# Performance work log

Hardware: AMD Instinct MI355X
Metric: run time of the kernel (lower is better)

Reference implementation:

```python
import jax, jax.numpy as jnp
import numpy as np
import math

B, CF, H, W = 2, 64, 256, 256
CH = 32          # 'channel' init arg
KS, DIL, PAD = 3, 2, 2
IMG_H, IMG_W = 512, 512


def _pos_encode(h, w, d_model):
    # Sinusoidal encoding along x and y, interleaved sin/cos -> [2*d_model, h, w]
    div = jnp.exp(jnp.arange(0, d_model, 2, dtype=jnp.float32) * (-math.log(10000.0) / d_model))  # [d/2]
    ax = jnp.arange(w, dtype=jnp.float32)[None, :] * div[:, None]   # [d/2, w]
    ay = jnp.arange(h, dtype=jnp.float32)[None, :] * div[:, None]   # [d/2, h]
    x = jnp.stack([jnp.sin(ax), jnp.cos(ax)], axis=1).reshape(d_model, w)  # even=sin, odd=cos
    y = jnp.stack([jnp.sin(ay), jnp.cos(ay)], axis=1).reshape(d_model, h)
    x = jnp.broadcast_to(x[:, None, :], (d_model, h, w))
    y = jnp.broadcast_to(y[:, :, None], (d_model, h, w))
    return jnp.concatenate([x, y], axis=0)  # [2*d_model, h, w]


def _unfold3x3(x):
    # F.unfold(kernel=3, dilation=2, padding=2, stride=1) -> [B, C, 9, H, W]
    b, c, h, w = x.shape
    xp = jnp.pad(x, ((0, 0), (0, 0), (PAD, PAD), (PAD, PAD)))
    offs = (0, DIL, 2 * DIL)
    patches = [xp[:, :, i:i + h, j:j + w] for i in offs for j in offs]  # row-major kernel order
    return jnp.stack(patches, axis=2)


def setup_inputs() -> dict:
    key = jax.random.key(0)
    k1, k2, k3, k4, k5 = jax.random.split(key, 5)
    return {
        "inp": jax.random.normal(k1, (B, CF, H, W), dtype=jnp.float32),
        "img": jax.random.uniform(k2, (B, 3, IMG_H, IMG_W), dtype=jnp.float32),
        "w_pos": jax.random.normal(k3, (CH, 2 * CH), dtype=jnp.float32) * 0.1,
        "w_img": jax.random.normal(k4, (CH, 3), dtype=jnp.float32) * 0.1,
        "w_comp": jax.random.normal(k5, (CF,), dtype=jnp.float32) * 0.1,
    }


def reference(inp, img, w_pos, w_img, w_comp):
    b, cf, h, w = inp.shape
    # positional embedding -> 1x1 conv (channel matmul)
    pos = _pos_encode(h, w, CH)                                   # [2*CH, H, W]
    pos_embd = jnp.einsum('oc,chw->ohw', w_pos, pos)              # [CH, H, W]
    pos_embd = jnp.broadcast_to(pos_embd[None], (b, CH, h, w))
    # bilinear resize of image to feature resolution, then 1x1 conv
    rimg = jax.image.resize(img, (b, 3, h, w), method='bilinear')
    rimg = jnp.einsum('oc,bchw->bohw', w_img, rimg)               # [B, CH, H, W]
    em = jnp.concatenate([rimg, pos_embd], axis=1)                # [B, 2*CH, H, W]
    # neighborhood similarity score
    un_em = _unfold3x3(em)                                        # [B, 2CH, 9, H, W]
    feature_score = jnp.einsum('bckhw,bchw->bkhw', un_em, em)     # [B, 9, H, W]
    # feature compatibility: 1x1 conv (dot with w_comp) per neighbor, sigmoid
    un_fea = _unfold3x3(inp)                                      # [B, CF, 9, H, W]
    comp_score = jax.nn.sigmoid(jnp.einsum('bckhw,c->bkhw', un_fea, w_comp))
    phi = comp_score * feature_score                              # [B, 9, H, W]
    weighted_fea = jnp.einsum('bckhw,bkhw->bchw', un_fea, phi)    # [B, CF, H, W]
    return weighted_fea
```

## Files before the change

### kernel.cpp

```cpp
#include <hip/hip_runtime.h>
#include <math.h>

namespace {
constexpr int Bn = 2, CF = 64;
constexpr int H = 256, W = 256, HW = H * W;
constexpr int IH = 512, IW = 512;

constexpr int OFF_MT   = 0;
constexpr int OFF_GXX  = OFF_MT + 256 * 256;
constexpr int OFF_GYY  = OFF_GXX + 3 * 256;
constexpr int OFF_G    = OFF_GYY + 3 * 256;
constexpr int OFF_RIMG = OFF_G + 16;
constexpr int OFF_S    = OFF_RIMG + Bn * 3 * HW;
constexpr int OFF_PX   = OFF_S + Bn * HW;
constexpr int OFF_PY   = OFF_PX + 32 * 256;

constexpr int GRAM_BLOCKS = 256;
constexpr int RIMG_BLOCKS = Bn * 3 * (HW / 256);
constexpr int SIGS_BLOCKS = Bn * (HW / 256);
constexpr int PREP_BLOCKS = GRAM_BLOCKS + RIMG_BLOCKS + SIGS_BLOCKS;
}

__global__ __launch_bounds__(256) void pxy_kernel(
    const float* __restrict__ w_pos,
    float* __restrict__ PX, float* __restrict__ PY)
{
  const int t = threadIdx.x;
  const int o = blockIdx.x;
  float s[16], c[16];
#pragma unroll
  for (int i = 0; i < 16; i++) {
    float d = expf((float)(2 * i) * (-0.2878231366242557f));
    float a = (float)t * d;
    s[i] = sinf(a);
    c[i] = cosf(a);
  }
  const float* wr = w_pos + o * 64;
  float ax = 0.f, ay = 0.f;
#pragma unroll
  for (int i = 0; i < 16; i++) {
    ax += wr[2 * i] * s[i] + wr[2 * i + 1] * c[i];
    ay += wr[32 + 2 * i] * s[i] + wr[33 + 2 * i] * c[i];
  }
  PX[o * 256 + t] = ax;
  PY[o * 256 + t] = ay;
}

__device__ __forceinline__ void resize_taps(int p, int n, float w[4], int idx[4])
{
#pragma unroll
  for (int r = 0; r < 4; r++) {
    int q = 2 * p - 1 + r;
    idx[r] = min(max(q, 0), 2 * n - 1);
  }
  if (p == 0)          { w[0] = 0.f;        w[1] = 3.f / 7.f; w[2] = 3.f / 7.f; w[3] = 1.f / 7.f; }
  else if (p == n - 1) { w[0] = 1.f / 7.f;  w[1] = 3.f / 7.f; w[2] = 3.f / 7.f; w[3] = 0.f; }
  else                 { w[0] = 0.125f;     w[1] = 0.375f;    w[2] = 0.375f;    w[3] = 0.125f; }
}

__global__ __launch_bounds__(256) void prep_kernel(
    const float* __restrict__ img, const float* __restrict__ inp,
    const float* __restrict__ w_comp, const float* __restrict__ w_img,
    const float* __restrict__ PX, const float* __restrict__ PY,
    float* __restrict__ rimg, float* __restrict__ sigs,
    float* __restrict__ Mt, float* __restrict__ GXX, float* __restrict__ GYY,
    float* __restrict__ G)
{
  __shared__ float4 red4[256];
  const int gid = blockIdx.x;

  if (gid < GRAM_BLOCKS) {
    const int a = threadIdx.x;
    const int t = gid;

    float m = 0.f;
#pragma unroll
    for (int o = 0; o < 32; o++) m += PX[o * 256 + a] * PY[o * 256 + t];
    Mt[t * 256 + a] = m;

    if (t == 0) {
#pragma unroll
      for (int j = 0; j < 3; j++) {
        const int nb = a + 2 * (j - 1);
        float gx = 0.f, gy = 0.f;
        if (nb >= 0 && nb < 256) {
#pragma unroll
          for (int o = 0; o < 32; o++) {
            gx += PX[o * 256 + a] * PX[o * 256 + nb];
            gy += PY[o * 256 + a] * PY[o * 256 + nb];
          }
        }
        GXX[j * 256 + a] = gx;
        GYY[j * 256 + a] = gy;
      }
      if (a < 9) {
        const int i = a / 3, j = a % 3;
        float g = 0.f;
#pragma unroll
        for (int o = 0; o < 32; o++) g += w_img[o * 3 + i] * w_img[o * 3 + j];
        G[a] = g;
      }
    }
  } else if (gid < GRAM_BLOCKS + RIMG_BLOCKS) {
    const int rid = gid - GRAM_BLOCKS;
    const int b = rid / 768;
    const int rem = rid % 768;
    const int c = rem / 256;
    const int p = (rem % 256) * 256 + threadIdx.x;
    const int x = p & (W - 1);
    const int y = p >> 8;

    float wy[4], wx[4];
    int ry[4], rx[4];
    resize_taps(y, H, wy, ry);
    resize_taps(x, W, wx, rx);

    const float* ip = img + ((size_t)(b * 3 + c) * IH) * IW;
    float acc = 0.f;
#pragma unroll
    for (int r = 0; r < 4; r++) {
      const float* rowp = ip + ry[r] * IW;
      float rs = wx[0] * rowp[rx[0]] + wx[1] * rowp[rx[1]] +
                 wx[2] * rowp[rx[2]] + wx[3] * rowp[rx[3]];
      acc += wy[r] * rs;
    }
    rimg[((size_t)(b * 3 + c)) * HW + p] = acc;
  } else {
    const int sid = gid - (GRAM_BLOCKS + RIMG_BLOCKS);
    const int b = sid / (HW / 256);
    const int pblk = sid % (HW / 256);
    const int lane = threadIdx.x & 63;
    const int cg = threadIdx.x >> 6;
    const int p0 = pblk * 256 + lane * 4;

    const float* ib = inp + (size_t)b * CF * HW + (size_t)cg * 16 * HW + p0;
    float4 acc = {0.f, 0.f, 0.f, 0.f};
#pragma unroll
    for (int c = 0; c < 16; c++) {
      const float4 v = *reinterpret_cast<const float4*>(ib + (size_t)c * HW);
      const float wc = w_comp[cg * 16 + c];
      acc.x += v.x * wc; acc.y += v.y * wc;
      acc.z += v.z * wc; acc.w += v.w * wc;
    }
    red4[threadIdx.x] = acc;
    __syncthreads();
    if (threadIdx.x < 64) {
      const float4 a = red4[threadIdx.x];
      const float4 b1 = red4[threadIdx.x + 64];
      const float4 c1 = red4[threadIdx.x + 128];
      const float4 d = red4[threadIdx.x + 192];
      float4 s;
      s.x = (a.x + b1.x) + (c1.x + d.x);
      s.y = (a.y + b1.y) + (c1.y + d.y);
      s.z = (a.z + b1.z) + (c1.z + d.z);
      s.w = (a.w + b1.w) + (c1.w + d.w);
      s.x = 1.f / (1.f + expf(-s.x));
      s.y = 1.f / (1.f + expf(-s.y));
      s.z = 1.f / (1.f + expf(-s.z));
      s.w = 1.f / (1.f + expf(-s.w));
      *reinterpret_cast<float4*>(sigs + (size_t)b * HW +
                                 pblk * 256 + threadIdx.x * 4) = s;
    }
  }
}

__global__ __launch_bounds__(256) void phigather_kernel(
    const float* __restrict__ inp, const float* __restrict__ rimg,
    const float* __restrict__ sigs, const float* __restrict__ Mt,
    const float* __restrict__ GXX, const float* __restrict__ GYY,
    const float* __restrict__ G, float* __restrict__ out)
{
  const int cg = blockIdx.x;
  const int p0 = (blockIdx.y * 256 + threadIdx.x) * 4;
  const int b = blockIdx.z;
  const int x0 = p0 & (W - 1);
  const int y  = p0 >> 8;

  const int xl = max(x0 - 2, 0);
  const int xr = min(x0 + 4, W - 2);

  int rowoff[3];
  bool vrow[3];
#pragma unroll
  for (int ky = 0; ky < 3; ky++) {
    const int cy = y + 2 * (ky - 1);
    vrow[ky] = ((unsigned)cy < (unsigned)H);
    rowoff[ky] = min(max(cy, 0), H - 1) * W;
  }

  const float* rb = rimg + (size_t)b * 3 * HW;
  const float* sb = sigs + (size_t)b * HW;

  const float4 r0 = *reinterpret_cast<const float4*>(rb + p0);
  const float4 r1 = *reinterpret_cast<const float4*>(rb + HW + p0);
  const float4 r2 = *reinterpret_cast<const float4*>(rb + 2 * HW + p0);
  float4 t0, t1, t2;
  {
    const float g0 = G[0], g1 = G[1], g2 = G[2];
    const float g3 = G[3], g4 = G[4], g5 = G[5];
    const float g6 = G[6], g7 = G[7], g8 = G[8];
    t0.x = r0.x * g0 + r1.x * g3 + r2.x * g6;
    t0.y = r0.y * g0 + r1.y * g3 + r2.y * g6;
    t0.z = r0.z * g0 + r1.z * g3 + r2.z * g6;
    t0.w = r0.w * g0 + r1.w * g3 + r2.w * g6;
    t1.x = r0.x * g1 + r1.x * g4 + r2.x * g7;
    t1.y = r0.y * g1 + r1.y * g4 + r2.y * g7;
    t1.z = r0.z * g1 + r1.z * g4 + r2.z * g7;
    t1.w = r0.w * g1 + r1.w * g4 + r2.w * g7;
    t2.x = r0.x * g2 + r1.x * g5 + r2.x * g8;
    t2.y = r0.y * g2 + r1.y * g5 + r2.y * g8;
    t2.z = r0.z * g2 + r1.z * g5 + r2.z * g8;
    t2.w = r0.w * g2 + r1.w * g5 + r2.w * g8;
  }

  float mrow[8];
  {
    const float2 L = *reinterpret_cast<const float2*>(Mt + y * W + xl);
    const float4 C = *reinterpret_cast<const float4*>(Mt + y * W + x0);
    const float2 R = *reinterpret_cast<const float2*>(Mt + y * W + xr);
    mrow[0] = L.x; mrow[1] = L.y; mrow[2] = C.x; mrow[3] = C.y;
    mrow[4] = C.z; mrow[5] = C.w; mrow[6] = R.x; mrow[7] = R.y;
  }
  float4 gxxv[3];
#pragma unroll
  for (int kx = 0; kx < 3; kx++)
    gxxv[kx] = *reinterpret_cast<const float4*>(GXX + kx * 256 + x0);

  float4 ph[9];
#pragma unroll
  for (int ky = 0; ky < 3; ky++) {
    const int ro = rowoff[ky];
    float a0[8], a1[8], a2[8], as_[8];
    {
      const float2 L0 = *reinterpret_cast<const float2*>(rb + ro + xl);
      const float4 C0 = *reinterpret_cast<const float4*>(rb + ro + x0);
      const float2 R0 = *reinterpret_cast<const float2*>(rb + ro + xr);
      a0[0]=L0.x; a0[1]=L0.y; a0[2]=C0.x; a0[3]=C0.y;
      a0[4]=C0.z; a0[5]=C0.w; a0[6]=R0.x; a0[7]=R0.y;
      const float2 L1 = *reinterpret_cast<const float2*>(rb + HW + ro + xl);
      const float4 C1 = *reinterpret_cast<const float4*>(rb + HW + ro + x0);
      const float2 R1 = *reinterpret_cast<const float2*>(rb + HW + ro + xr);
      a1[0]=L1.x; a1[1]=L1.y; a1[2]=C1.x; a1[3]=C1.y;
      a1[4]=C1.z; a1[5]=C1.w; a1[6]=R1.x; a1[7]=R1.y;
      const float2 L2 = *reinterpret_cast<const float2*>(rb + 2 * HW + ro + xl);
      const float4 C2 = *reinterpret_cast<const float4*>(rb + 2 * HW + ro + x0);
      const float2 R2 = *reinterpret_cast<const float2*>(rb + 2 * HW + ro + xr);
      a2[0]=L2.x; a2[1]=L2.y; a2[2]=C2.x; a2[3]=C2.y;
      a2[4]=C2.z; a2[5]=C2.w; a2[6]=R2.x; a2[7]=R2.y;
      const float2 Ls = *reinterpret_cast<const float2*>(sb + ro + xl);
      const float4 Cs = *reinterpret_cast<const float4*>(sb + ro + x0);
      const float2 Rs = *reinterpret_cast<const float2*>(sb + ro + xr);
      as_[0]=Ls.x; as_[1]=Ls.y; as_[2]=Cs.x; as_[3]=Cs.y;
      as_[4]=Cs.z; as_[5]=Cs.w; as_[6]=Rs.x; as_[7]=Rs.y;
    }
    const float4 mc = *reinterpret_cast<const float4*>(Mt + ro + x0);
    const float gyy = GYY[ky * 256 + y];

#pragma unroll
    for (int kx = 0; kx < 3; kx++) {
      float4 p;
      {
        const int rel = 0 + 2 * kx;
        const float fs = t0.x * a0[rel] + t1.x * a1[rel] + t2.x * a2[rel]
                       + gxxv[kx].x + gyy + mrow[rel] + mc.x;
        const bool v = vrow[ky] && ((unsigned)(x0 + 0 + 2 * (kx - 1)) < (unsigned)W);
        p.x = v ? as_[rel] * fs : 0.f;
      }
      {
        const int rel = 1 + 2 * kx;
        const float fs = t0.y * a0[rel] + t1.y * a1[rel] + t2.y * a2[rel]
                       + gxxv[kx].y + gyy + mrow[rel] + mc.y;
        const bool v = vrow[ky] && ((unsigned)(x0 + 1 + 2 * (kx - 1)) < (unsigned)W);
        p.y = v ? as_[rel] * fs : 0.f;
      }
      {
        const int rel = 2 + 2 * kx;
        const float fs = t0.z * a0[rel] + t1.z * a1[rel] + t2.z * a2[rel]
                       + gxxv[kx].z + gyy + mrow[rel] + mc.z;
        const bool v = vrow[ky] && ((unsigned)(x0 + 2 + 2 * (kx - 1)) < (unsigned)W);
        p.z = v ? as_[rel] * fs : 0.f;
      }
      {
        const int rel = 3 + 2 * kx;
        const float fs = t0.w * a0[rel] + t1.w * a1[rel] + t2.w * a2[rel]
                       + gxxv[kx].w + gyy + mrow[rel] + mc.w;
        const bool v = vrow[ky] && ((unsigned)(x0 + 3 + 2 * (kx - 1)) < (unsigned)W);
        p.w = v ? as_[rel] * fs : 0.f;
      }
      ph[ky * 3 + kx] = p;
    }
  }

  const float* ib = inp + ((size_t)b * CF + cg * 8) * HW;
  float* ob = out + ((size_t)b * CF + cg * 8) * HW + p0;
#pragma unroll 4
  for (int c = 0; c < 8; c++) {
    const float* ic = ib + (size_t)c * HW;
    float4 acc = {0.f, 0.f, 0.f, 0.f};
#pragma unroll
    for (int ky = 0; ky < 3; ky++) {
      const int ro = rowoff[ky];
      const float2 L = *reinterpret_cast<const float2*>(ic + ro + xl);
      const float4 C = *reinterpret_cast<const float4*>(ic + ro + x0);
      const float2 R = *reinterpret_cast<const float2*>(ic + ro + xr);
      const float a[8] = {L.x, L.y, C.x, C.y, C.z, C.w, R.x, R.y};
#pragma unroll
      for (int kx = 0; kx < 3; kx++) {
        const float4 w = ph[ky * 3 + kx];
        acc.x += w.x * a[0 + 2 * kx];
        acc.y += w.y * a[1 + 2 * kx];
        acc.z += w.z * a[2 + 2 * kx];
        acc.w += w.w * a[3 + 2 * kx];
      }
    }
    *reinterpret_cast<float4*>(ob + (size_t)c * HW) = acc;
  }
}

extern "C" void kernel_launch(void* const* d_in, const int* in_sizes, int n_in,
                              void* d_out, int out_size, void* d_ws, size_t ws_size,
                              hipStream_t stream)
{
  const float* inp    = (const float*)d_in[0];
  const float* img    = (const float*)d_in[1];
  const float* w_pos  = (const float*)d_in[2];
  const float* w_img  = (const float*)d_in[3];
  const float* w_comp = (const float*)d_in[4];
  float* out = (float*)d_out;
  float* ws  = (float*)d_ws;

  float* Mt   = ws + OFF_MT;
  float* GXX  = ws + OFF_GXX;
  float* GYY  = ws + OFF_GYY;
  float* G    = ws + OFF_G;
  float* rimg = ws + OFF_RIMG;
  float* sigs = ws + OFF_S;
  float* PX   = ws + OFF_PX;
  float* PY   = ws + OFF_PY;

  hipLaunchKernelGGL(pxy_kernel, dim3(32), dim3(256), 0, stream, w_pos, PX, PY);

  hipLaunchKernelGGL(prep_kernel, dim3(PREP_BLOCKS), dim3(256), 0, stream,
                     img, inp, w_comp, w_img, PX, PY,
                     rimg, sigs, Mt, GXX, GYY, G);

  hipLaunchKernelGGL(phigather_kernel, dim3(8, HW / 1024, Bn), dim3(256), 0, stream,
                     inp, rimg, sigs, Mt, GXX, GYY, G, out);
}
```

Measured before the change: 118.6 us.

## Fold positional projection into prep kernel via w_pos Gram matrices

Removes the separate pxy_kernel launch that materialised the projected positional tables PX/PY. Each gram block now loads w_pos into shared memory and forms 32x32 Gram matrices of its x/y halves. It then rebuilds Mt and the GXX/GYY neighbour terms directly from sinusoid bases, which drops one kernel launch and the dependency between kernels. In exchange, every gram block recomputes the small Gram matrix and many sin/cos values redundantly, and block 0 carries a heavier serial workload.

```diff
diff --git a/kernel.cpp b/kernel.cpp
--- a/kernel.cpp
+++ b/kernel.cpp
@@ -12,38 +12,13 @@
 constexpr int OFF_G    = OFF_GYY + 3 * 256;
 constexpr int OFF_RIMG = OFF_G + 16;
 constexpr int OFF_S    = OFF_RIMG + Bn * 3 * HW;
-constexpr int OFF_PX   = OFF_S + Bn * HW;
-constexpr int OFF_PY   = OFF_PX + 32 * 256;
 
 constexpr int GRAM_BLOCKS = 256;
 constexpr int RIMG_BLOCKS = Bn * 3 * (HW / 256);
 constexpr int SIGS_BLOCKS = Bn * (HW / 256);
 constexpr int PREP_BLOCKS = GRAM_BLOCKS + RIMG_BLOCKS + SIGS_BLOCKS;
-}
-
-__global__ __launch_bounds__(256) void pxy_kernel(
-    const float* __restrict__ w_pos,
-    float* __restrict__ PX, float* __restrict__ PY)
-{
-  const int t = threadIdx.x;
-  const int o = blockIdx.x;
-  float s[16], c[16];
-#pragma unroll
-  for (int i = 0; i < 16; i++) {
-    float d = expf((float)(2 * i) * (-0.2878231366242557f));
-    float a = (float)t * d;
-    s[i] = sinf(a);
-    c[i] = cosf(a);
-  }
-  const float* wr = w_pos + o * 64;
-  float ax = 0.f, ay = 0.f;
-#pragma unroll
-  for (int i = 0; i < 16; i++) {
-    ax += wr[2 * i] * s[i] + wr[2 * i + 1] * c[i];
-    ay += wr[32 + 2 * i] * s[i] + wr[33 + 2 * i] * c[i];
-  }
-  PX[o * 256 + t] = ax;
-  PY[o * 256 + t] = ay;
+
+constexpr float DEXP = -0.2878231366242557f;
 }
 
 __device__ __forceinline__ void resize_taps(int p, int n, float w[4], int idx[4])
@@ -61,38 +36,119 @@
 __global__ __launch_bounds__(256) void prep_kernel(
     const float* __restrict__ img, const float* __restrict__ inp,
     const float* __restrict__ w_comp, const float* __restrict__ w_img,
-    const float* __restrict__ PX, const float* __restrict__ PY,
+    const float* __restrict__ w_pos,
     float* __restrict__ rimg, float* __restrict__ sigs,
     float* __restrict__ Mt, float* __restrict__ GXX, float* __restrict__ GYY,
     float* __restrict__ G)
 {
-  __shared__ float4 red4[256];
+  __shared__ __align__(16) float smem[5152];
   const int gid = blockIdx.x;
 
   if (gid < GRAM_BLOCKS) {
+    float* wp  = smem;
+    float* Ks  = smem + 2048;
+    float* KXs = smem + 3072;
+    float* KYs = smem + 4096;
+    float* wv  = smem + 5120;
     const int a = threadIdx.x;
     const int t = gid;
 
+#pragma unroll
+    for (int i = 0; i < 8; i++) wp[i * 256 + a] = w_pos[i * 256 + a];
+    __syncthreads();
+
+    const int Ki = a >> 3;
+    const int Kj0 = (a & 7) * 4;
+    {
+      float k0 = 0.f, k1 = 0.f, k2 = 0.f, k3 = 0.f;
+#pragma unroll
+      for (int o = 0; o < 32; o++) {
+        const float xe = wp[o * 64 + Ki];
+        const float* yo = wp + o * 64 + 32;
+        k0 += xe * yo[Kj0 + 0];
+        k1 += xe * yo[Kj0 + 1];
+        k2 += xe * yo[Kj0 + 2];
+        k3 += xe * yo[Kj0 + 3];
+      }
+      Ks[Ki * 32 + Kj0 + 0] = k0;
+      Ks[Ki * 32 + Kj0 + 1] = k1;
+      Ks[Ki * 32 + Kj0 + 2] = k2;
+      Ks[Ki * 32 + Kj0 + 3] = k3;
+    }
+    if (t == 0) {
+      float x0 = 0.f, x1 = 0.f, x2 = 0.f, x3 = 0.f;
+      float y0 = 0.f, y1 = 0.f, y2 = 0.f, y3 = 0.f;
+#pragma unroll
+      for (int o = 0; o < 32; o++) {
+        const float xe = wp[o * 64 + Ki];
+        const float ye = wp[o * 64 + 32 + Ki];
+        const float* xo = wp + o * 64;
+        const float* yo = wp + o * 64 + 32;
+        x0 += xe * xo[Kj0 + 0]; x1 += xe * xo[Kj0 + 1];
+        x2 += xe * xo[Kj0 + 2]; x3 += xe * xo[Kj0 + 3];
+        y0 += ye * yo[Kj0 + 0]; y1 += ye * yo[Kj0 + 1];
+        y2 += ye * yo[Kj0 + 2]; y3 += ye * yo[Kj0 + 3];
+      }
+      KXs[Ki * 32 + Kj0 + 0] = x0; KXs[Ki * 32 + Kj0 + 1] = x1;
+      KXs[Ki * 32 + Kj0 + 2] = x2; KXs[Ki * 32 + Kj0 + 3] = x3;
+      KYs[Ki * 32 + Kj0 + 0] = y0; KYs[Ki * 32 + Kj0 + 1] = y1;
+      KYs[Ki * 32 + Kj0 + 2] = y2; KYs[Ki * 32 + Kj0 + 3] = y3;
+    }
+    __syncthreads();
+
+    if (a < 32) {
+      float acc = 0.f;
+#pragma unroll
+      for (int i = 0; i < 16; i++) {
+        const float d = expf((float)(2 * i) * DEXP);
+        const float ang = (float)t * d;
+        acc += Ks[a * 32 + 2 * i] * sinf(ang) + Ks[a * 32 + 2 * i + 1] * cosf(ang);
+      }
+      wv[a] = acc;
+    }
+    __syncthreads();
+
+    float sa[16], ca[16];
+#pragma unroll
+    for (int i = 0; i < 16; i++) {
+      const float d = expf((float)(2 * i) * DEXP);
+      const float ang = (float)a * d;
+      sa[i] = sinf(ang);
+      ca[i] = cosf(ang);
+    }
     float m = 0.f;
 #pragma unroll
-    for (int o = 0; o < 32; o++) m += PX[o * 256 + a] * PY[o * 256 + t];
+    for (int i = 0; i < 16; i++) m += wv[2 * i] * sa[i] + wv[2 * i + 1] * ca[i];
     Mt[t * 256 + a] = m;
 
     if (t == 0) {
-#pragma unroll
-      for (int j = 0; j < 3; j++) {
-        const int nb = a + 2 * (j - 1);
-        float gx = 0.f, gy = 0.f;
-        if (nb >= 0 && nb < 256) {
-#pragma unroll
-          for (int o = 0; o < 32; o++) {
-            gx += PX[o * 256 + a] * PX[o * 256 + nb];
-            gy += PY[o * 256 + a] * PY[o * 256 + nb];
-          }
+      float gx0 = 0.f, gx1 = 0.f, gx2 = 0.f;
+      float gy0 = 0.f, gy1 = 0.f, gy2 = 0.f;
+#pragma unroll
+      for (int i = 0; i < 16; i++) {
+        const float d = expf((float)(2 * i) * DEXP);
+        float zxs = 0.f, zxc = 0.f, zys = 0.f, zyc = 0.f;
+#pragma unroll
+        for (int f = 0; f < 16; f++) {
+          zxs += KXs[(2 * i) * 32 + 2 * f] * sa[f] + KXs[(2 * i) * 32 + 2 * f + 1] * ca[f];
+          zxc += KXs[(2 * i + 1) * 32 + 2 * f] * sa[f] + KXs[(2 * i + 1) * 32 + 2 * f + 1] * ca[f];
+          zys += KYs[(2 * i) * 32 + 2 * f] * sa[f] + KYs[(2 * i) * 32 + 2 * f + 1] * ca[f];
+          zyc += KYs[(2 * i + 1) * 32 + 2 * f] * sa[f] + KYs[(2 * i + 1) * 32 + 2 * f + 1] * ca[f];
         }
-        GXX[j * 256 + a] = gx;
-        GYY[j * 256 + a] = gy;
-      }
+        const float am = (float)(a - 2) * d, ap = (float)(a + 2) * d;
+        const float sm = sinf(am), cm = cosf(am);
+        const float sp = sinf(ap), cp = cosf(ap);
+        gx0 += sm * zxs + cm * zxc;  gy0 += sm * zys + cm * zyc;
+        gx1 += sa[i] * zxs + ca[i] * zxc;  gy1 += sa[i] * zys + ca[i] * zyc;
+        gx2 += sp * zxs + cp * zxc;  gy2 += sp * zys + cp * zyc;
+      }
+      const bool vm = (a - 2) >= 0, vp = (a + 2) < 256;
+      GXX[0 * 256 + a] = vm ? gx0 : 0.f;
+      GXX[1 * 256 + a] = gx1;
+      GXX[2 * 256 + a] = vp ? gx2 : 0.f;
+      GYY[0 * 256 + a] = vm ? gy0 : 0.f;
+      GYY[1 * 256 + a] = gy1;
+      GYY[2 * 256 + a] = vp ? gy2 : 0.f;
       if (a < 9) {
         const int i = a / 3, j = a % 3;
         float g = 0.f;
@@ -126,6 +182,7 @@
     }
     rimg[((size_t)(b * 3 + c)) * HW + p] = acc;
   } else {
+    float4* red4 = reinterpret_cast<float4*>(smem);
     const int sid = gid - (GRAM_BLOCKS + RIMG_BLOCKS);
     const int b = sid / (HW / 256);
     const int pblk = sid % (HW / 256);
@@ -335,13 +392,9 @@
   float* G    = ws + OFF_G;
   float* rimg = ws + OFF_RIMG;
   float* sigs = ws + OFF_S;
-  float* PX   = ws + OFF_PX;
-  float* PY   = ws + OFF_PY;
-
-  hipLaunchKernelGGL(pxy_kernel, dim3(32), dim3(256), 0, stream, w_pos, PX, PY);
 
   hipLaunchKernelGGL(prep_kernel, dim3(PREP_BLOCKS), dim3(256), 0, stream,
-                     img, inp, w_comp, w_img, PX, PY,
+                     img, inp, w_comp, w_img, w_pos,
                      rimg, sigs, Mt, GXX, GYY, G);
 
   hipLaunchKernelGGL(phigather_kernel, dim3(8, HW / 1024, Bn), dim3(256), 0, stream,
```

New measurement: 262.7 us. 2.21x slower.
